# Performance work log

Measured on AMD Instinct MI355X. Metric: run time of the kernel, lower is better.

## Reference

```python
import jax, jax.numpy as jnp
import numpy as np
import math

COND_DIM = 64
HIDDEN = 128
NUM_SIN = 2
SQRT2 = 1.4142135623730951


def fused_leaky_relu(x, bias):
    # stylegan2 fused bias + leaky relu (slope 0.2) with sqrt(2) gain
    return jax.nn.leaky_relu(x + bias, negative_slope=0.2) * SQRT2


def equal_linear2(x, W, b, lr_mul=1.0, activation=False):
    scale = lr_mul / math.sqrt(W.shape[1])
    out = x @ (W * scale).T
    if activation:
        return fused_leaky_relu(out, b * lr_mul)
    return out + b * lr_mul


def coords_to_sinusoidals(x, num_sinusoidals=NUM_SIN, multiplier=2.0):
    # x: [P, 1] -> [P, 2*num_sinusoidals], freq_type='mult': freqs = multiplier**i
    freqs = multiplier ** jnp.arange(num_sinusoidals, dtype=x.dtype)  # [S]
    ang = x * freqs  # [P, S]
    return jnp.concatenate([jnp.sin(ang), jnp.cos(ang)], axis=-1)


def setup_inputs() -> dict:
    key = jax.random.key(0)
    ks = jax.random.split(key, 10)
    B, N = 64, 8192
    coord_in = 2 * NUM_SIN  # 4
    in1 = coord_in + COND_DIM  # 68
    in2 = HIDDEN + COND_DIM    # 192
    coords = jax.random.normal(ks[0], (B, N, 2), dtype=jnp.float32)
    c = jax.random.normal(ks[1], (B, N, COND_DIM), dtype=jnp.float32)
    # EqualLinear2 weights init uniform(-1,1)/lr_mul; last layer zero in torch,
    # use small random values here so gradients/outputs are non-trivial.
    Wx1 = jax.random.uniform(ks[2], (HIDDEN, in1), minval=-1.0, maxval=1.0)
    bx1 = jnp.zeros((HIDDEN,), jnp.float32)
    Wx2 = jax.random.uniform(ks[3], (2, in2), minval=-1.0, maxval=1.0) * 0.1
    bx2 = jnp.zeros((2,), jnp.float32)
    Wy1 = jax.random.uniform(ks[4], (HIDDEN, in1), minval=-1.0, maxval=1.0)
    by1 = jnp.zeros((HIDDEN,), jnp.float32)
    Wy2 = jax.random.uniform(ks[5], (2, in2), minval=-1.0, maxval=1.0) * 0.1
    by2 = jnp.zeros((2,), jnp.float32)
    return {"coords": coords, "c": c,
            "Wx1": Wx1, "bx1": bx1, "Wx2": Wx2, "bx2": bx2,
            "Wy1": Wy1, "by1": by1, "Wy2": Wy2, "by2": by2}


def reference(coords, c, Wx1, bx1, Wx2, bx2, Wy1, by1, Wy2, by2):
    initial_shape = coords.shape[:-1]
    coords2 = coords.reshape(-1, coords.shape[-1])  # [P, 2]
    cf = c.reshape(-1, c.shape[-1])                 # [P, cond]
    x = coords2[:, 0:1]
    y = coords2[:, 1:2]

    # x branch -> affine params for y
    h = coords_to_sinusoidals(x / 10.0)
    h = equal_linear2(jnp.concatenate([h, cf], -1), Wx1, bx1, activation=True)
    o = equal_linear2(jnp.concatenate([h, cf], -1), Wx2, bx2, activation=False)
    y_log_scale = jnp.clip(o[:, 0:1], -5.0, 5.0)
    y_bias = o[:, 1:2]
    y = y * jnp.exp(y_log_scale) + y_bias

    # y branch -> affine params for x
    h = coords_to_sinusoidals(y / 10.0)
    h = equal_linear2(jnp.concatenate([h, cf], -1), Wy1, by1, activation=True)
    o = equal_linear2(jnp.concatenate([h, cf], -1), Wy2, by2, activation=False)
    x_log_scale = jnp.clip(o[:, 0:1], -5.0, 5.0)
    x_bias = o[:, 1:2]
    x = x * jnp.exp(x_log_scale) + x_bias

    warped = jnp.concatenate([x, y], -1).reshape(*initial_shape, -1)
    log_jac = jnp.concatenate([x_log_scale + y_log_scale], -1)
    log_jac = (x_log_scale + y_log_scale).reshape(*initial_shape, -1)
    return warped, log_jac
```

## Files before the change

kernel.cpp:

```cpp
#include <hip/hip_runtime.h>

typedef unsigned short u16t;
typedef short short8 __attribute__((ext_vector_type(8)));
typedef float f32x4 __attribute__((ext_vector_type(4)));

__device__ __forceinline__ u16t f2bf(float f) {
  unsigned int u = __builtin_bit_cast(unsigned int, f);
  u += 0x7FFFu + ((u >> 16) & 1u);
  return (u16t)(u >> 16);
}
__device__ __forceinline__ ushort4 cvt4(float4 v) {
  ushort4 r;
  r.x = f2bf(v.x); r.y = f2bf(v.y); r.z = f2bf(v.z); r.w = f2bf(v.w);
  return r;
}
__device__ __forceinline__ short8 pack8(ushort4 a, ushort4 b) {
  short8 r;
  r[0] = (short)a.x; r[1] = (short)a.y; r[2] = (short)a.z; r[3] = (short)a.w;
  r[4] = (short)b.x; r[5] = (short)b.y; r[6] = (short)b.z; r[7] = (short)b.w;
  return r;
}

#define LDS_WX1 0
#define LDS_WY1 8704
#define LDS_W2C 17408
#define FP_STRIDE 528

__global__ __launch_bounds__(256, 2)
void icb_kernel(const float* __restrict__ g_coords, const float* __restrict__ g_c,
                const float* __restrict__ g_Wx1, const float* __restrict__ g_bx1,
                const float* __restrict__ g_Wx2, const float* __restrict__ g_bx2,
                const float* __restrict__ g_Wy1, const float* __restrict__ g_by1,
                const float* __restrict__ g_Wy2, const float* __restrict__ g_by2,
                float* __restrict__ g_out)
{
  __shared__ __align__(16) u16t  c_lds[256 * 72];
  __shared__ __align__(16) u16t  w_lds[17664];
  __shared__ __align__(16) float f_lds[1056];
  __shared__ __align__(16) float2 xy_lds[256];

  const int tid  = threadIdx.x;
  const int row0 = blockIdx.x * 256;

  #pragma unroll
  for (int it = 0; it < 16; ++it) {
    int i = it * 256 + tid;
    int r = i >> 4, o = i & 15;
    float4 v = reinterpret_cast<const float4*>(g_c)[(size_t)(row0 + r) * 16 + o];
    *reinterpret_cast<ushort4*>(&c_lds[r * 72 + o * 4]) = cvt4(v);
  }
  xy_lds[tid] = reinterpret_cast<const float2*>(g_coords)[row0 + tid];
  for (int i = tid; i < 2176; i += 256) {
    *reinterpret_cast<ushort4*>(&w_lds[LDS_WX1 + i * 4]) =
        cvt4(reinterpret_cast<const float4*>(g_Wx1)[i]);
    *reinterpret_cast<ushort4*>(&w_lds[LDS_WY1 + i * 4]) =
        cvt4(reinterpret_cast<const float4*>(g_Wy1)[i]);
  }
  {
    int p = tid >> 7, t = tid & 127, o = t >> 6, k = t & 63;
    const float* W2 = p ? g_Wy2 : g_Wx2;
    w_lds[LDS_W2C + p * 128 + o * 64 + k] = f2bf(W2[o * 192 + 128 + k]);
  }
  {
    float4* f4 = reinterpret_cast<float4*>(f_lds);
    if (tid < 32)                f4[tid]       = reinterpret_cast<const float4*>(g_bx1)[tid];
    if (tid >= 32 && tid < 128)  f4[tid]       = reinterpret_cast<const float4*>(g_Wx2)[tid - 32];
    if (tid >= 128 && tid < 160) f4[4 + tid]   = reinterpret_cast<const float4*>(g_by1)[tid - 128];
    if (tid >= 160)              f4[4 + tid]   = reinterpret_cast<const float4*>(g_Wy2)[tid - 160];
    if (tid == 0) { f_lds[512]  = g_bx2[0]; f_lds[513]  = g_bx2[1]; }
    if (tid == 1) { f_lds[FP_STRIDE + 512] = g_by2[0]; f_lds[FP_STRIDE + 513] = g_by2[1]; }
  }
  __syncthreads();

  const int lane = tid & 63;
  const int wave = tid >> 6;
  const int l15  = lane & 15;
  const int quad = lane >> 4;
  const int wrow = wave * 64;

  float xold[4], yold[4];
  #pragma unroll
  for (int mt = 0; mt < 4; ++mt) {
    float2 p = xy_lds[wrow + mt * 16 + l15];
    xold[mt] = p.x;  yold[mt] = p.y;
  }

  short8 aC0[4], aC1[4];
  #pragma unroll
  for (int mt = 0; mt < 4; ++mt) {
    const int r = wrow + mt * 16 + l15;
    aC0[mt] = *reinterpret_cast<const short8*>(&c_lds[r * 72 + quad * 8]);
    aC1[mt] = *reinterpret_cast<const short8*>(&c_lds[r * 72 + 32 + quad * 8]);
  }

  const float s1  = 0.121267812518166f;
  const float s2  = 0.0721687836487032f;
  const float SQ2 = 1.41421356237309515f;

  float vin[4], ynew[4], xnew[4], yls[4], xls[4];
  #pragma unroll
  for (int mt = 0; mt < 4; ++mt) vin[mt] = xold[mt];

  #pragma unroll 1
  for (int path = 0; path < 2; ++path) {
    const u16t*  W1  = w_lds + (path ? LDS_WY1 : LDS_WX1);
    const u16t*  W2C = w_lds + LDS_W2C + path * 128;
    const float* F   = f_lds + path * FP_STRIDE;
    const float b20 = F[512], b21 = F[513];

    short8 aS[4];
    #pragma unroll
    for (int mt = 0; mt < 4; ++mt) {
      short8 f = (short8)0;
      if (quad == 0) {
        float a = vin[mt] * 0.1f;
        float sa, ca;
        __sincosf(a, &sa, &ca);
        float s2a = 2.0f * sa * ca;
        float c2a = 1.0f - 2.0f * sa * sa;
        f[0] = (short)f2bf(sa);  f[1] = (short)f2bf(s2a);
        f[2] = (short)f2bf(ca);  f[3] = (short)f2bf(c2a);
      }
      aS[mt] = f;
    }

    float hp[4][4][2];
    #pragma unroll
    for (int mt = 0; mt < 4; ++mt)
      #pragma unroll
      for (int j = 0; j < 4; ++j) { hp[mt][j][0] = 0.f; hp[mt][j][1] = 0.f; }

    #pragma unroll 1
    for (int nt = 0; nt < 8; ++nt) {
      const int n = nt * 16 + l15;
      const u16t* rp = W1 + n * 68;
      ushort4 q0 = *reinterpret_cast<const ushort4*>(rp + 4  + quad * 8);
      ushort4 q1 = *reinterpret_cast<const ushort4*>(rp + 8  + quad * 8);
      ushort4 q2 = *reinterpret_cast<const ushort4*>(rp + 36 + quad * 8);
      ushort4 q3 = *reinterpret_cast<const ushort4*>(rp + 40 + quad * 8);
      short8 bb0 = pack8(q0, q1);
      short8 bb1 = pack8(q2, q3);
      short8 bs = (short8)0;
      if (quad == 0) {
        ushort4 h = *reinterpret_cast<const ushort4*>(rp);
        bs[0] = (short)h.x; bs[1] = (short)h.y; bs[2] = (short)h.z; bs[3] = (short)h.w;
      }
      const float b1v = F[n];
      const float w20 = F[128 + n] * SQ2;
      const float w21 = F[128 + 192 + n] * SQ2;

      #pragma unroll
      for (int mt = 0; mt < 4; ++mt) {
        f32x4 acc = {0.f, 0.f, 0.f, 0.f};
        acc = __builtin_amdgcn_mfma_f32_16x16x32_bf16(aC0[mt], bb0, acc, 0, 0, 0);
        acc = __builtin_amdgcn_mfma_f32_16x16x32_bf16(aC1[mt], bb1, acc, 0, 0, 0);
        acc = __builtin_amdgcn_mfma_f32_16x16x32_bf16(aS[mt],  bs,  acc, 0, 0, 0);
        #pragma unroll
        for (int j = 0; j < 4; ++j) {
          float v = fmaf(s1, acc[j], b1v);
          float h = fmaxf(v, 0.2f * v);
          hp[mt][j][0] = fmaf(h, w20, hp[mt][j][0]);
          hp[mt][j][1] = fmaf(h, w21, hp[mt][j][1]);
        }
      }
    }

    short8 bc0 = (short8)0, bc1 = (short8)0;
    if (l15 < 2) {
      const u16t* r2 = W2C + l15 * 64;
      ushort4 p0 = *reinterpret_cast<const ushort4*>(r2 + quad * 8);
      ushort4 p1 = *reinterpret_cast<const ushort4*>(r2 + 4 + quad * 8);
      ushort4 p2 = *reinterpret_cast<const ushort4*>(r2 + 32 + quad * 8);
      ushort4 p3 = *reinterpret_cast<const ushort4*>(r2 + 36 + quad * 8);
      bc0 = pack8(p0, p1);
      bc1 = pack8(p2, p3);
    }
    f32x4 acc8[4];
    #pragma unroll
    for (int mt = 0; mt < 4; ++mt) {
      f32x4 a = {0.f, 0.f, 0.f, 0.f};
      a = __builtin_amdgcn_mfma_f32_16x16x32_bf16(aC0[mt], bc0, a, 0, 0, 0);
      a = __builtin_amdgcn_mfma_f32_16x16x32_bf16(aC1[mt], bc1, a, 0, 0, 0);
      acc8[mt] = a;
    }

    #pragma unroll
    for (int mt = 0; mt < 4; ++mt)
      #pragma unroll
      for (int j = 0; j < 4; ++j)
        #pragma unroll
        for (int o = 0; o < 2; ++o) {
          float v = hp[mt][j][o];
          v += __shfl_xor(v, 1);
          v += __shfl_xor(v, 2);
          v += __shfl_xor(v, 4);
          v += __shfl_xor(v, 8);
          hp[mt][j][o] = v;
        }

    const int qsrc = (l15 >> 2) << 4;
    const int jm   = l15 & 3;
    #pragma unroll
    for (int mt = 0; mt < 4; ++mt) {
      float t0[4], t1[4];
      #pragma unroll
      for (int j = 0; j < 4; ++j) {
        float cp0 = __shfl(acc8[mt][j], (lane & 48));
        float cp1 = __shfl(acc8[mt][j], (lane & 48) | 1);
        t0[j] = fmaf(s2, hp[mt][j][0] + cp0, b20);
        t1[j] = fmaf(s2, hp[mt][j][1] + cp1, b21);
      }
      float u0 = __shfl(t0[0], qsrc), u1 = __shfl(t0[1], qsrc),
            u2 = __shfl(t0[2], qsrc), u3 = __shfl(t0[3], qsrc);
      float lsraw = (jm == 0) ? u0 : (jm == 1) ? u1 : (jm == 2) ? u2 : u3;
      float v0 = __shfl(t1[0], qsrc), v1 = __shfl(t1[1], qsrc),
            v2 = __shfl(t1[2], qsrc), v3 = __shfl(t1[3], qsrc);
      float brow = (jm == 0) ? v0 : (jm == 1) ? v1 : (jm == 2) ? v2 : v3;

      float ls = fminf(fmaxf(lsraw, -5.f), 5.f);
      float e  = __expf(ls);
      if (path == 0) {
        yls[mt]  = ls;
        ynew[mt] = fmaf(yold[mt], e, brow);
        vin[mt]  = ynew[mt];
      } else {
        xls[mt]  = ls;
        xnew[mt] = fmaf(xold[mt], e, brow);
      }
    }
  }

  if (lane < 16) {
    #pragma unroll
    for (int mt = 0; mt < 4; ++mt) {
      int R = row0 + wrow + mt * 16 + lane;
      float2 pw; pw.x = xnew[mt]; pw.y = ynew[mt];
      reinterpret_cast<float2*>(g_out)[R] = pw;
      g_out[1048576 + R] = xls[mt] + yls[mt];
    }
  }
}

extern "C" void kernel_launch(void* const* d_in, const int* in_sizes, int n_in,
                              void* d_out, int out_size, void* d_ws, size_t ws_size,
                              hipStream_t stream) {
  (void)in_sizes; (void)n_in; (void)out_size; (void)d_ws; (void)ws_size;
  icb_kernel<<<2048, 256, 0, stream>>>(
      (const float*)d_in[0], (const float*)d_in[1],
      (const float*)d_in[2], (const float*)d_in[3],
      (const float*)d_in[4], (const float*)d_in[5],
      (const float*)d_in[6], (const float*)d_in[7],
      (const float*)d_in[8], (const float*)d_in[9],
      (float*)d_out);
}
```

Baseline: 267.0 us.

## Pre-swizzle weights into MFMA fragments in workspace and drop LDS staging

Adds a one-block prep kernel that converts the layer weights to bf16 once per call and stores them in the exact per-lane MFMA fragment layout, with bias and second-layer scale packed as float4. The main kernel stops converting weights into LDS in every block and loads these fragments directly from global/L2. It also reads c straight from global into registers, uses no shared memory or barrier, halves rows per wave to raise occupancy, folds the c-part of layer two into the shuffle reduction, and cuts the broadcast shuffles. The cost is an extra kernel launch, repeated per-lane global weight loads that rely on cache hits, and truncating round-to-nearest bf16 packing of c.

Result: faster. 240.8 us (-9.8%).

```diff
diff --git a/kernel.cpp b/kernel.cpp
--- a/kernel.cpp
+++ b/kernel.cpp
@@ -4,113 +4,120 @@
 typedef short short8 __attribute__((ext_vector_type(8)));
 typedef float f32x4 __attribute__((ext_vector_type(4)));
 
-__device__ __forceinline__ u16t f2bf(float f) {
-  unsigned int u = __builtin_bit_cast(unsigned int, f);
+__device__ __forceinline__ u16t f2bf_rne(float f) {
+  unsigned u = __builtin_bit_cast(unsigned, f);
   u += 0x7FFFu + ((u >> 16) & 1u);
   return (u16t)(u >> 16);
 }
-__device__ __forceinline__ ushort4 cvt4(float4 v) {
-  ushort4 r;
-  r.x = f2bf(v.x); r.y = f2bf(v.y); r.z = f2bf(v.z); r.w = f2bf(v.w);
-  return r;
-}
-__device__ __forceinline__ short8 pack8(ushort4 a, ushort4 b) {
-  short8 r;
-  r[0] = (short)a.x; r[1] = (short)a.y; r[2] = (short)a.z; r[3] = (short)a.w;
-  r[4] = (short)b.x; r[5] = (short)b.y; r[6] = (short)b.z; r[7] = (short)b.w;
-  return r;
-}
-
-#define LDS_WX1 0
-#define LDS_WY1 8704
-#define LDS_W2C 17408
-#define FP_STRIDE 528
-
-__global__ __launch_bounds__(256, 2)
-void icb_kernel(const float* __restrict__ g_coords, const float* __restrict__ g_c,
-                const float* __restrict__ g_Wx1, const float* __restrict__ g_bx1,
-                const float* __restrict__ g_Wx2, const float* __restrict__ g_bx2,
-                const float* __restrict__ g_Wy1, const float* __restrict__ g_by1,
-                const float* __restrict__ g_Wy2, const float* __restrict__ g_by2,
-                float* __restrict__ g_out)
+__device__ __forceinline__ unsigned pk2(float a, float b) {
+  unsigned ua = __builtin_bit_cast(unsigned, a) + 0x8000u;
+  unsigned ub = __builtin_bit_cast(unsigned, b) + 0x8000u;
+  return (ua >> 16) | (ub & 0xFFFF0000u);
+}
+union S8U { short8 s; unsigned w[4]; };
+__device__ __forceinline__ short8 pack8f(float4 a, float4 b) {
+  S8U u;
+  u.w[0] = pk2(a.x, a.y); u.w[1] = pk2(a.z, a.w);
+  u.w[2] = pk2(b.x, b.y); u.w[3] = pk2(b.z, b.w);
+  return u.s;
+}
+
+#define WS_WB  0
+#define WS_BS  32768
+#define WS_FF  49152
+#define WS_BC  65536
+
+__global__ void prep_kernel(const float* __restrict__ Wx1, const float* __restrict__ bx1,
+                            const float* __restrict__ Wx2,
+                            const float* __restrict__ Wy1, const float* __restrict__ by1,
+                            const float* __restrict__ Wy2,
+                            char* __restrict__ ws)
 {
-  __shared__ __align__(16) u16t  c_lds[256 * 72];
-  __shared__ __align__(16) u16t  w_lds[17664];
-  __shared__ __align__(16) float f_lds[1056];
-  __shared__ __align__(16) float2 xy_lds[256];
-
+  const int tid = threadIdx.x;
+  const int p = tid >> 9, nt = (tid >> 6) & 7, lane = tid & 63;
+  const int l15 = lane & 15, quad = lane >> 4;
+  const float* W1 = p ? Wy1 : Wx1;
+  const float* B1 = p ? by1 : bx1;
+  const float* W2 = p ? Wy2 : Wx2;
+  const int n = nt * 16 + l15;
+  const float* rp = W1 + n * 68;
+  short8 bb0, bb1, bs = (short8)0;
+  #pragma unroll
+  for (int j = 0; j < 8; ++j) {
+    bb0[j] = (short)f2bf_rne(rp[4 + quad * 8 + j]);
+    bb1[j] = (short)f2bf_rne(rp[36 + quad * 8 + j]);
+  }
+  if (quad == 0) {
+    #pragma unroll
+    for (int j = 0; j < 4; ++j) bs[j] = (short)f2bf_rne(rp[j]);
+  }
+  short8* wb = (short8*)(ws + WS_WB);
+  wb[((p * 8 + nt) * 2 + 0) * 64 + lane] = bb0;
+  wb[((p * 8 + nt) * 2 + 1) * 64 + lane] = bb1;
+  ((short8*)(ws + WS_BS))[(p * 8 + nt) * 64 + lane] = bs;
+  const float SQ2 = 1.41421356237309515f;
+  float4 ff;
+  ff.x = B1[n]; ff.y = W2[n] * SQ2; ff.z = W2[192 + n] * SQ2; ff.w = 0.f;
+  ((float4*)(ws + WS_FF))[(p * 8 + nt) * 64 + lane] = ff;
+
+  if (tid < 256) {
+    const int p2 = tid >> 7, h = (tid >> 6) & 1, ln = tid & 63;
+    const int l2 = ln & 15, q2 = ln >> 4;
+    const float* W2b = p2 ? Wy2 : Wx2;
+    short8 bc = (short8)0;
+    if (l2 < 2) {
+      #pragma unroll
+      for (int j = 0; j < 8; ++j)
+        bc[j] = (short)f2bf_rne(W2b[l2 * 192 + 128 + h * 32 + q2 * 8 + j]);
+    }
+    ((short8*)(ws + WS_BC))[(p2 * 2 + h) * 64 + ln] = bc;
+  }
+}
+
+__global__ __launch_bounds__(256, 4)
+void icb_main(const float* __restrict__ g_coords, const float* __restrict__ g_c,
+              const float* __restrict__ g_bx2, const float* __restrict__ g_by2,
+              const char* __restrict__ ws, float* __restrict__ g_out)
+{
   const int tid  = threadIdx.x;
-  const int row0 = blockIdx.x * 256;
-
+  const int lane = tid & 63, wave = tid >> 6;
+  const int l15  = lane & 15, quad = lane >> 4;
+  const int wbase = blockIdx.x * 128 + wave * 32;
+
+  const short8* wb  = (const short8*)(ws + WS_WB);
+  const short8* wbs = (const short8*)(ws + WS_BS);
+  const float4* wf  = (const float4*)(ws + WS_FF);
+  const short8* wbc = (const short8*)(ws + WS_BC);
+
+  short8 aC0[2], aC1[2];
+  float xold[2], yold[2];
   #pragma unroll
-  for (int it = 0; it < 16; ++it) {
-    int i = it * 256 + tid;
-    int r = i >> 4, o = i & 15;
-    float4 v = reinterpret_cast<const float4*>(g_c)[(size_t)(row0 + r) * 16 + o];
-    *reinterpret_cast<ushort4*>(&c_lds[r * 72 + o * 4]) = cvt4(v);
-  }
-  xy_lds[tid] = reinterpret_cast<const float2*>(g_coords)[row0 + tid];
-  for (int i = tid; i < 2176; i += 256) {
-    *reinterpret_cast<ushort4*>(&w_lds[LDS_WX1 + i * 4]) =
-        cvt4(reinterpret_cast<const float4*>(g_Wx1)[i]);
-    *reinterpret_cast<ushort4*>(&w_lds[LDS_WY1 + i * 4]) =
-        cvt4(reinterpret_cast<const float4*>(g_Wy1)[i]);
-  }
-  {
-    int p = tid >> 7, t = tid & 127, o = t >> 6, k = t & 63;
-    const float* W2 = p ? g_Wy2 : g_Wx2;
-    w_lds[LDS_W2C + p * 128 + o * 64 + k] = f2bf(W2[o * 192 + 128 + k]);
-  }
-  {
-    float4* f4 = reinterpret_cast<float4*>(f_lds);
-    if (tid < 32)                f4[tid]       = reinterpret_cast<const float4*>(g_bx1)[tid];
-    if (tid >= 32 && tid < 128)  f4[tid]       = reinterpret_cast<const float4*>(g_Wx2)[tid - 32];
-    if (tid >= 128 && tid < 160) f4[4 + tid]   = reinterpret_cast<const float4*>(g_by1)[tid - 128];
-    if (tid >= 160)              f4[4 + tid]   = reinterpret_cast<const float4*>(g_Wy2)[tid - 160];
-    if (tid == 0) { f_lds[512]  = g_bx2[0]; f_lds[513]  = g_bx2[1]; }
-    if (tid == 1) { f_lds[FP_STRIDE + 512] = g_by2[0]; f_lds[FP_STRIDE + 513] = g_by2[1]; }
-  }
-  __syncthreads();
-
-  const int lane = tid & 63;
-  const int wave = tid >> 6;
-  const int l15  = lane & 15;
-  const int quad = lane >> 4;
-  const int wrow = wave * 64;
-
-  float xold[4], yold[4];
-  #pragma unroll
-  for (int mt = 0; mt < 4; ++mt) {
-    float2 p = xy_lds[wrow + mt * 16 + l15];
-    xold[mt] = p.x;  yold[mt] = p.y;
-  }
-
-  short8 aC0[4], aC1[4];
-  #pragma unroll
-  for (int mt = 0; mt < 4; ++mt) {
-    const int r = wrow + mt * 16 + l15;
-    aC0[mt] = *reinterpret_cast<const short8*>(&c_lds[r * 72 + quad * 8]);
-    aC1[mt] = *reinterpret_cast<const short8*>(&c_lds[r * 72 + 32 + quad * 8]);
-  }
-
-  const float s1  = 0.121267812518166f;
-  const float s2  = 0.0721687836487032f;
-  const float SQ2 = 1.41421356237309515f;
-
-  float vin[4], ynew[4], xnew[4], yls[4], xls[4];
-  #pragma unroll
-  for (int mt = 0; mt < 4; ++mt) vin[mt] = xold[mt];
+  for (int mt = 0; mt < 2; ++mt) {
+    const int r = wbase + mt * 16 + l15;
+    const float4* cr = (const float4*)(g_c + (size_t)r * 64);
+    float4 a0 = cr[quad * 2],     a1 = cr[quad * 2 + 1];
+    float4 a2 = cr[8 + quad * 2], a3 = cr[8 + quad * 2 + 1];
+    aC0[mt] = pack8f(a0, a1);
+    aC1[mt] = pack8f(a2, a3);
+    float2 p = ((const float2*)g_coords)[r];
+    xold[mt] = p.x; yold[mt] = p.y;
+  }
+
+  const float s1 = 0.121267812518166f;
+  const float s2 = 0.0721687836487032f;
+
+  float vin[2], xnew[2], ynew[2], xls[2], yls[2];
+  vin[0] = xold[0]; vin[1] = xold[1];
 
   #pragma unroll 1
   for (int path = 0; path < 2; ++path) {
-    const u16t*  W1  = w_lds + (path ? LDS_WY1 : LDS_WX1);
-    const u16t*  W2C = w_lds + LDS_W2C + path * 128;
-    const float* F   = f_lds + path * FP_STRIDE;
-    const float b20 = F[512], b21 = F[513];
-
-    short8 aS[4];
-    #pragma unroll
-    for (int mt = 0; mt < 4; ++mt) {
+    const int pb = path * 8;
+    const float* b2 = path ? g_by2 : g_bx2;
+    const float b20 = b2[0], b21 = b2[1];
+
+    short8 aS[2];
+    #pragma unroll
+    for (int mt = 0; mt < 2; ++mt) {
       short8 f = (short8)0;
       if (quad == 0) {
         float a = vin[mt] * 0.1f;
@@ -118,74 +125,61 @@
         __sincosf(a, &sa, &ca);
         float s2a = 2.0f * sa * ca;
         float c2a = 1.0f - 2.0f * sa * sa;
-        f[0] = (short)f2bf(sa);  f[1] = (short)f2bf(s2a);
-        f[2] = (short)f2bf(ca);  f[3] = (short)f2bf(c2a);
+        f[0] = (short)f2bf_rne(sa); f[1] = (short)f2bf_rne(s2a);
+        f[2] = (short)f2bf_rne(ca); f[3] = (short)f2bf_rne(c2a);
       }
       aS[mt] = f;
     }
 
-    float hp[4][4][2];
-    #pragma unroll
-    for (int mt = 0; mt < 4; ++mt)
+    short8 bc0 = wbc[(path * 2 + 0) * 64 + lane];
+    short8 bc1 = wbc[(path * 2 + 1) * 64 + lane];
+    f32x4 acc8[2];
+    #pragma unroll
+    for (int mt = 0; mt < 2; ++mt) {
+      f32x4 a = {0.f, 0.f, 0.f, 0.f};
+      a = __builtin_amdgcn_mfma_f32_16x16x32_bf16(aC0[mt], bc0, a, 0, 0, 0);
+      a = __builtin_amdgcn_mfma_f32_16x16x32_bf16(aC1[mt], bc1, a, 0, 0, 0);
+      acc8[mt] = a;
+    }
+
+    float hp[2][4][2];
+    #pragma unroll
+    for (int mt = 0; mt < 2; ++mt)
       #pragma unroll
       for (int j = 0; j < 4; ++j) { hp[mt][j][0] = 0.f; hp[mt][j][1] = 0.f; }
 
-    #pragma unroll 1
+    #pragma unroll 2
     for (int nt = 0; nt < 8; ++nt) {
-      const int n = nt * 16 + l15;
-      const u16t* rp = W1 + n * 68;
-      ushort4 q0 = *reinterpret_cast<const ushort4*>(rp + 4  + quad * 8);
-      ushort4 q1 = *reinterpret_cast<const ushort4*>(rp + 8  + quad * 8);
-      ushort4 q2 = *reinterpret_cast<const ushort4*>(rp + 36 + quad * 8);
-      ushort4 q3 = *reinterpret_cast<const ushort4*>(rp + 40 + quad * 8);
-      short8 bb0 = pack8(q0, q1);
-      short8 bb1 = pack8(q2, q3);
-      short8 bs = (short8)0;
-      if (quad == 0) {
-        ushort4 h = *reinterpret_cast<const ushort4*>(rp);
-        bs[0] = (short)h.x; bs[1] = (short)h.y; bs[2] = (short)h.z; bs[3] = (short)h.w;
-      }
-      const float b1v = F[n];
-      const float w20 = F[128 + n] * SQ2;
-      const float w21 = F[128 + 192 + n] * SQ2;
-
-      #pragma unroll
-      for (int mt = 0; mt < 4; ++mt) {
+      short8 bb0 = wb[((pb + nt) * 2 + 0) * 64 + lane];
+      short8 bb1 = wb[((pb + nt) * 2 + 1) * 64 + lane];
+      short8 bs  = wbs[(pb + nt) * 64 + lane];
+      float4 ff  = wf[(pb + nt) * 64 + lane];
+      #pragma unroll
+      for (int mt = 0; mt < 2; ++mt) {
         f32x4 acc = {0.f, 0.f, 0.f, 0.f};
         acc = __builtin_amdgcn_mfma_f32_16x16x32_bf16(aC0[mt], bb0, acc, 0, 0, 0);
         acc = __builtin_amdgcn_mfma_f32_16x16x32_bf16(aC1[mt], bb1, acc, 0, 0, 0);
         acc = __builtin_amdgcn_mfma_f32_16x16x32_bf16(aS[mt],  bs,  acc, 0, 0, 0);
         #pragma unroll
         for (int j = 0; j < 4; ++j) {
-          float v = fmaf(s1, acc[j], b1v);
+          float v = fmaf(s1, acc[j], ff.x);
           float h = fmaxf(v, 0.2f * v);
-          hp[mt][j][0] = fmaf(h, w20, hp[mt][j][0]);
-          hp[mt][j][1] = fmaf(h, w21, hp[mt][j][1]);
+          hp[mt][j][0] = fmaf(h, ff.y, hp[mt][j][0]);
+          hp[mt][j][1] = fmaf(h, ff.z, hp[mt][j][1]);
         }
       }
     }
 
-    short8 bc0 = (short8)0, bc1 = (short8)0;
-    if (l15 < 2) {
-      const u16t* r2 = W2C + l15 * 64;
-      ushort4 p0 = *reinterpret_cast<const ushort4*>(r2 + quad * 8);
-      ushort4 p1 = *reinterpret_cast<const ushort4*>(r2 + 4 + quad * 8);
-      ushort4 p2 = *reinterpret_cast<const ushort4*>(r2 + 32 + quad * 8);
-      ushort4 p3 = *reinterpret_cast<const ushort4*>(r2 + 36 + quad * 8);
-      bc0 = pack8(p0, p1);
-      bc1 = pack8(p2, p3);
-    }
-    f32x4 acc8[4];
-    #pragma unroll
-    for (int mt = 0; mt < 4; ++mt) {
-      f32x4 a = {0.f, 0.f, 0.f, 0.f};
-      a = __builtin_amdgcn_mfma_f32_16x16x32_bf16(aC0[mt], bc0, a, 0, 0, 0);
-      a = __builtin_amdgcn_mfma_f32_16x16x32_bf16(aC1[mt], bc1, a, 0, 0, 0);
-      acc8[mt] = a;
-    }
-
-    #pragma unroll
-    for (int mt = 0; mt < 4; ++mt)
+    #pragma unroll
+    for (int mt = 0; mt < 2; ++mt)
+      #pragma unroll
+      for (int j = 0; j < 4; ++j) {
+        hp[mt][j][0] += (l15 == 0) ? acc8[mt][j] : 0.f;
+        hp[mt][j][1] += (l15 == 1) ? acc8[mt][j] : 0.f;
+      }
+
+    #pragma unroll
+    for (int mt = 0; mt < 2; ++mt)
       #pragma unroll
       for (int j = 0; j < 4; ++j)
         #pragma unroll
@@ -198,24 +192,22 @@
           hp[mt][j][o] = v;
         }
 
-    const int qsrc = (l15 >> 2) << 4;
-    const int jm   = l15 & 3;
-    #pragma unroll
-    for (int mt = 0; mt < 4; ++mt) {
+    const int jm = l15 & 3;
+    const int src = ((l15 >> 2) << 4) | jm;
+    #pragma unroll
+    for (int mt = 0; mt < 2; ++mt) {
       float t0[4], t1[4];
       #pragma unroll
       for (int j = 0; j < 4; ++j) {
-        float cp0 = __shfl(acc8[mt][j], (lane & 48));
-        float cp1 = __shfl(acc8[mt][j], (lane & 48) | 1);
-        t0[j] = fmaf(s2, hp[mt][j][0] + cp0, b20);
-        t1[j] = fmaf(s2, hp[mt][j][1] + cp1, b21);
-      }
-      float u0 = __shfl(t0[0], qsrc), u1 = __shfl(t0[1], qsrc),
-            u2 = __shfl(t0[2], qsrc), u3 = __shfl(t0[3], qsrc);
-      float lsraw = (jm == 0) ? u0 : (jm == 1) ? u1 : (jm == 2) ? u2 : u3;
-      float v0 = __shfl(t1[0], qsrc), v1 = __shfl(t1[1], qsrc),
-            v2 = __shfl(t1[2], qsrc), v3 = __shfl(t1[3], qsrc);
-      float brow = (jm == 0) ? v0 : (jm == 1) ? v1 : (jm == 2) ? v2 : v3;
+        t0[j] = fmaf(s2, hp[mt][j][0], b20);
+        t1[j] = fmaf(s2, hp[mt][j][1], b21);
+      }
+      float s0 = (jm & 1) ? t0[1] : t0[0], s0b = (jm & 1) ? t0[3] : t0[2];
+      s0 = (jm & 2) ? s0b : s0;
+      float s1v = (jm & 1) ? t1[1] : t1[0], s1b = (jm & 1) ? t1[3] : t1[2];
+      s1v = (jm & 2) ? s1b : s1v;
+      float lsraw = __shfl(s0, src);
+      float brow  = __shfl(s1v, src);
 
       float ls = fminf(fmaxf(lsraw, -5.f), 5.f);
       float e  = __expf(ls);
@@ -232,8 +224,8 @@
 
   if (lane < 16) {
     #pragma unroll
-    for (int mt = 0; mt < 4; ++mt) {
-      int R = row0 + wrow + mt * 16 + lane;
+    for (int mt = 0; mt < 2; ++mt) {
+      int R = wbase + mt * 16 + lane;
       float2 pw; pw.x = xnew[mt]; pw.y = ynew[mt];
       reinterpret_cast<float2*>(g_out)[R] = pw;
       g_out[1048576 + R] = xls[mt] + yls[mt];
@@ -244,12 +236,13 @@
 extern "C" void kernel_launch(void* const* d_in, const int* in_sizes, int n_in,
                               void* d_out, int out_size, void* d_ws, size_t ws_size,
                               hipStream_t stream) {
-  (void)in_sizes; (void)n_in; (void)out_size; (void)d_ws; (void)ws_size;
-  icb_kernel<<<2048, 256, 0, stream>>>(
+  (void)in_sizes; (void)n_in; (void)out_size; (void)ws_size;
+  prep_kernel<<<1, 1024, 0, stream>>>(
+      (const float*)d_in[2], (const float*)d_in[3], (const float*)d_in[4],
+      (const float*)d_in[6], (const float*)d_in[7], (const float*)d_in[8],
+      (char*)d_ws);
+  icb_main<<<4096, 256, 0, stream>>>(
       (const float*)d_in[0], (const float*)d_in[1],
-      (const float*)d_in[2], (const float*)d_in[3],
-      (const float*)d_in[4], (const float*)d_in[5],
-      (const float*)d_in[6], (const float*)d_in[7],
-      (const float*)d_in[8], (const float*)d_in[9],
-      (float*)d_out);
-}
+      (const float*)d_in[5], (const float*)d_in[9],
+      (const char*)d_ws, (float*)d_out);
+}
```
